# Kernel tuning notes

Hardware: AMD Instinct MI355X
Metric: run time of the kernel (lower is better)

Reference implementation:

```python
import jax, jax.numpy as jnp
import numpy as np

TOKEN_DIM = 1024
HIDDEN = 256
NUM_FREQS = 10
FOURIER_DIM = 3 * (2 * NUM_FREQS + 1)  # include_input + sin/cos per freq = 63
EPS_LN = 1e-5
EPS_NORM = 1e-12


def fourier_encode(x):
    # x: [..., 3] -> [..., 3*(1+2*NUM_FREQS)]
    freqs = (2.0 ** jnp.arange(NUM_FREQS)).astype(x.dtype)  # [F]
    xf = x[..., None] * freqs  # [..., 3, F]
    sin = jnp.sin(xf)
    cos = jnp.cos(xf)
    enc = jnp.concatenate([x[..., None], sin, cos], axis=-1)  # [..., 3, 1+2F]
    return enc.reshape(*x.shape[:-1], FOURIER_DIM)


def layer_norm(x, g, b):
    mu = jnp.mean(x, axis=-1, keepdims=True)
    var = jnp.mean((x - mu) ** 2, axis=-1, keepdims=True)
    return (x - mu) * jax.lax.rsqrt(var + EPS_LN) * g + b


def setup_inputs() -> dict:
    key = jax.random.key(0)
    ks = jax.random.split(key, 12)
    B, T, N = 2, 512, 40000
    in_dim = TOKEN_DIM + FOURIER_DIM
    s1 = 1.0 / np.sqrt(in_dim)
    s2 = 1.0 / np.sqrt(HIDDEN)
    return {
        "transformer_tokens": jax.random.normal(ks[0], (B, T, TOKEN_DIM), jnp.float32),
        "scaffold_anchors": jax.random.normal(ks[1], (B, T, 3), jnp.float32),
        "scaffold_token_ids": jax.random.randint(ks[2], (B, N), 0, T, jnp.int32),
        "W1": jax.random.uniform(ks[3], (in_dim, HIDDEN), jnp.float32, -s1, s1),
        "b1": jnp.zeros((HIDDEN,), jnp.float32),
        "g1": jnp.ones((HIDDEN,), jnp.float32),
        "be1": jnp.zeros((HIDDEN,), jnp.float32),
        "W2": jax.random.uniform(ks[4], (HIDDEN, HIDDEN), jnp.float32, -s2, s2),
        "b2": jnp.zeros((HIDDEN,), jnp.float32),
        "g2": jnp.ones((HIDDEN,), jnp.float32),
        "be2": jnp.zeros((HIDDEN,), jnp.float32),
        "W3": jax.random.uniform(ks[5], (HIDDEN, 14), jnp.float32, -s2, s2),
        "b3": jnp.zeros((14,), jnp.float32),
    }


def reference(transformer_tokens, scaffold_anchors, scaffold_token_ids,
              W1, b1, g1, be1, W2, b2, g2, be2, W3, b3):
    B, T, D = transformer_tokens.shape
    N = scaffold_token_ids.shape[1]
    idx = scaffold_token_ids.astype(jnp.int32)
    # Gather per-Gaussian anchors and token features: [B, N, 3] / [B, N, D]
    per_anchor = jnp.take_along_axis(scaffold_anchors, idx[..., None], axis=1)
    token_feats = jnp.take_along_axis(transformer_tokens, idx[..., None], axis=1)
    spatial_enc = fourier_encode(per_anchor)  # [B, N, FOURIER_DIM]
    combined = jnp.concatenate([token_feats, spatial_enc], axis=-1)
    h = jax.nn.relu(layer_norm(combined @ W1 + b1, g1, be1))
    h = jax.nn.relu(layer_norm(h @ W2 + b2, g2, be2))
    raw = h @ W3 + b3  # [B, N, 14]
    pos = raw[..., 0:3]
    color = jnp.clip(raw[..., 3:6], 0.0, 1.0)
    opac = jax.nn.sigmoid(raw[..., 6:7])
    scale = jnp.exp(raw[..., 7:10])
    q = raw[..., 10:14]
    qn = jnp.linalg.norm(q, axis=-1, keepdims=True)
    quat = q / jnp.maximum(qn, EPS_NORM)
    out = jnp.concatenate([pos, color, opac, scale, quat], axis=-1)
    return out.reshape(B, N * 14)
```

## Files before the change

kernel.cpp:

```cpp
#include <hip/hip_runtime.h>

#define TDIM   1024
#define HID    256
#define FDIM   63
#define INDIM  1087
#define TT     512
#define NBATCH 2
#define NROWS  1024
#define KSPLIT 4
#define KCHUNK 272
#define EPS_LN   1e-5f
#define EPS_NORM 1e-12f

#define FMA4(A, s, W)                                   \
    (A).x = fmaf((s), (W).x, (A).x);                    \
    (A).y = fmaf((s), (W).y, (A).y);                    \
    (A).z = fmaf((s), (W).z, (A).z);                    \
    (A).w = fmaf((s), (W).w, (A).w)

__device__ __forceinline__ float wave_reduce_sum(float v) {
    #pragma unroll
    for (int m = 32; m >= 1; m >>= 1) v += __shfl_xor(v, m);
    return v;
}

__device__ __forceinline__ float fourier_val(const float* __restrict__ anchors, int row, int u) {
    const int c = u / 21;
    const int w = u % 21;
    const float x = anchors[row * 3 + c];
    if (w == 0)  return x;
    if (w <= 10) return sinf(x * (float)(1u << (w - 1)));
    return cosf(x * (float)(1u << (w - 11)));
}

__global__ __launch_bounds__(512) void stage1_partial_kernel(
    const float* __restrict__ tokens,
    const float* __restrict__ anchors,
    const float* __restrict__ W1,
    float* __restrict__ part)
{
    const int tid    = threadIdx.x;
    const int rt     = blockIdx.x >> 2;
    const int z      = blockIdx.x & 3;
    const int kstart = z * KCHUNK;
    const int kcount = min(KCHUNK, INDIM - kstart);
    const int wave   = tid >> 6;
    const int c4     = (tid & 63) << 2;
    const int row0   = rt * 16 + wave * 2;

    const float* __restrict__ t0p = tokens + (size_t)(row0 + 0) * TDIM;
    const float* __restrict__ t1p = tokens + (size_t)(row0 + 1) * TDIM;

    float4 acc0 = {0.f, 0.f, 0.f, 0.f};
    float4 acc1 = acc0;

    const int glim = kcount >> 2;
    const int gtok = (kstart < TDIM) ? min(glim, (TDIM - kstart) >> 2) : 0;

    #pragma unroll 4
    for (int g = 0; g < gtok; ++g) {
        const int k = kstart + (g << 2);
        const float4 w0 = *(const float4*)&W1[(size_t)(k + 0) * HID + c4];
        const float4 w1 = *(const float4*)&W1[(size_t)(k + 1) * HID + c4];
        const float4 w2 = *(const float4*)&W1[(size_t)(k + 2) * HID + c4];
        const float4 w3 = *(const float4*)&W1[(size_t)(k + 3) * HID + c4];
        const float4 s0 = *(const float4*)&t0p[k];
        const float4 s1 = *(const float4*)&t1p[k];
        FMA4(acc0, s0.x, w0); FMA4(acc0, s0.y, w1); FMA4(acc0, s0.z, w2); FMA4(acc0, s0.w, w3);
        FMA4(acc1, s1.x, w0); FMA4(acc1, s1.y, w1); FMA4(acc1, s1.z, w2); FMA4(acc1, s1.w, w3);
    }

    for (int g = gtok; g < glim; ++g) {
        const int k = kstart + (g << 2);
        const float4 w0 = *(const float4*)&W1[(size_t)(k + 0) * HID + c4];
        const float4 w1 = *(const float4*)&W1[(size_t)(k + 1) * HID + c4];
        const float4 w2 = *(const float4*)&W1[(size_t)(k + 2) * HID + c4];
        const float4 w3 = *(const float4*)&W1[(size_t)(k + 3) * HID + c4];
        const int u = k - TDIM;
        float4 s0, s1;
        s0.x = fourier_val(anchors, row0 + 0, u);     s0.y = fourier_val(anchors, row0 + 0, u + 1);
        s0.z = fourier_val(anchors, row0 + 0, u + 2); s0.w = fourier_val(anchors, row0 + 0, u + 3);
        s1.x = fourier_val(anchors, row0 + 1, u);     s1.y = fourier_val(anchors, row0 + 1, u + 1);
        s1.z = fourier_val(anchors, row0 + 1, u + 2); s1.w = fourier_val(anchors, row0 + 1, u + 3);
        FMA4(acc0, s0.x, w0); FMA4(acc0, s0.y, w1); FMA4(acc0, s0.z, w2); FMA4(acc0, s0.w, w3);
        FMA4(acc1, s1.x, w0); FMA4(acc1, s1.y, w1); FMA4(acc1, s1.z, w2); FMA4(acc1, s1.w, w3);
    }

    for (int k = kstart + (glim << 2); k < kstart + kcount; ++k) {
        const float4 w = *(const float4*)&W1[(size_t)k * HID + c4];
        const float v0 = (k < TDIM) ? t0p[k] : fourier_val(anchors, row0 + 0, k - TDIM);
        const float v1 = (k < TDIM) ? t1p[k] : fourier_val(anchors, row0 + 1, k - TDIM);
        FMA4(acc0, v0, w); FMA4(acc1, v1, w);
    }

    float* __restrict__ pb = part + (size_t)z * NROWS * HID;
    *(float4*)&pb[(size_t)(row0 + 0) * HID + c4] = acc0;
    *(float4*)&pb[(size_t)(row0 + 1) * HID + c4] = acc1;
}

__global__ __launch_bounds__(256) void decode_tail_kernel(
    const float* __restrict__ part,
    const float* __restrict__ b1,
    const float* __restrict__ g1,
    const float* __restrict__ be1,
    const float* __restrict__ W2,
    const float* __restrict__ b2,
    const float* __restrict__ g2,
    const float* __restrict__ be2,
    const float* __restrict__ W3,
    const float* __restrict__ b3,
    float* __restrict__ decoded)
{
    __shared__ float h1[4][HID];
    __shared__ float h2[4][HID];
    __shared__ float raws[4][16];

    const int tid  = threadIdx.x;
    const int wave = tid >> 6;
    const int lane = tid & 63;
    const int row  = blockIdx.x * 4 + wave;

    {
        const size_t off = (size_t)row * HID;
        float x0 = b1[lane], x1 = b1[lane + 64], x2 = b1[lane + 128], x3 = b1[lane + 192];
        #pragma unroll
        for (int zz = 0; zz < KSPLIT; ++zz) {
            const float* __restrict__ p = part + (size_t)zz * NROWS * HID + off;
            x0 += p[lane]; x1 += p[lane + 64]; x2 += p[lane + 128]; x3 += p[lane + 192];
        }
        const float ga0 = g1[lane], ga1 = g1[lane + 64], ga2 = g1[lane + 128], ga3 = g1[lane + 192];
        const float bb0 = be1[lane], bb1 = be1[lane + 64], bb2 = be1[lane + 128], bb3 = be1[lane + 192];
        const float s  = wave_reduce_sum(x0 + x1 + x2 + x3);
        const float mu = s * (1.0f / 256.0f);
        const float d0 = x0 - mu, d1 = x1 - mu, d2 = x2 - mu, d3 = x3 - mu;
        const float sq = wave_reduce_sum(d0 * d0 + d1 * d1 + d2 * d2 + d3 * d3);
        const float rstd = 1.0f / sqrtf(sq * (1.0f / 256.0f) + EPS_LN);
        h1[wave][lane]       = fmaxf(0.0f, fmaf(d0 * rstd, ga0, bb0));
        h1[wave][lane + 64]  = fmaxf(0.0f, fmaf(d1 * rstd, ga1, bb1));
        h1[wave][lane + 128] = fmaxf(0.0f, fmaf(d2 * rstd, ga2, bb2));
        h1[wave][lane + 192] = fmaxf(0.0f, fmaf(d3 * rstd, ga3, bb3));
    }
    __syncthreads();

    {
        const int cc = lane << 2;
        float4 acc = *(const float4*)&b2[cc];
        #pragma unroll 4
        for (int k = 0; k < HID; k += 4) {
            const float4 hk = *(const float4*)&h1[wave][k];
            const float4 w0 = *(const float4*)&W2[(size_t)(k + 0) * HID + cc];
            const float4 w1 = *(const float4*)&W2[(size_t)(k + 1) * HID + cc];
            const float4 w2 = *(const float4*)&W2[(size_t)(k + 2) * HID + cc];
            const float4 w3 = *(const float4*)&W2[(size_t)(k + 3) * HID + cc];
            FMA4(acc, hk.x, w0); FMA4(acc, hk.y, w1); FMA4(acc, hk.z, w2); FMA4(acc, hk.w, w3);
        }
        *(float4*)&h2[wave][cc] = acc;
    }
    __syncthreads();

    {
        float x0 = h2[wave][lane], x1 = h2[wave][lane + 64], x2 = h2[wave][lane + 128], x3 = h2[wave][lane + 192];
        const float ga0 = g2[lane], ga1 = g2[lane + 64], ga2 = g2[lane + 128], ga3 = g2[lane + 192];
        const float bb0 = be2[lane], bb1 = be2[lane + 64], bb2 = be2[lane + 128], bb3 = be2[lane + 192];
        const float s  = wave_reduce_sum(x0 + x1 + x2 + x3);
        const float mu = s * (1.0f / 256.0f);
        const float d0 = x0 - mu, d1 = x1 - mu, d2 = x2 - mu, d3 = x3 - mu;
        const float sq = wave_reduce_sum(d0 * d0 + d1 * d1 + d2 * d2 + d3 * d3);
        const float rstd = 1.0f / sqrtf(sq * (1.0f / 256.0f) + EPS_LN);
        h2[wave][lane]       = fmaxf(0.0f, fmaf(d0 * rstd, ga0, bb0));
        h2[wave][lane + 64]  = fmaxf(0.0f, fmaf(d1 * rstd, ga1, bb1));
        h2[wave][lane + 128] = fmaxf(0.0f, fmaf(d2 * rstd, ga2, bb2));
        h2[wave][lane + 192] = fmaxf(0.0f, fmaf(d3 * rstd, ga3, bb3));
    }
    __syncthreads();

    if (tid < 4 * 14) {
        const int r = tid / 14;
        const int m = tid % 14;
        float a = b3[m];
        #pragma unroll 4
        for (int k = 0; k < HID; ++k) a = fmaf(h2[r][k], W3[k * 14 + m], a);
        raws[r][m] = a;
    }
    __syncthreads();

    if (tid < 4 * 14) {
        const int r = tid / 14;
        const int m = tid % 14;
        const float x = raws[r][m];
        float v;
        if (m < 3) {
            v = x;
        } else if (m < 6) {
            v = fminf(fmaxf(x, 0.0f), 1.0f);
        } else if (m == 6) {
            v = 1.0f / (1.0f + expf(-x));
        } else if (m < 10) {
            v = expf(x);
        } else {
            const float q0 = raws[r][10], q1 = raws[r][11];
            const float q2 = raws[r][12], q3 = raws[r][13];
            const float nrm = sqrtf(q0 * q0 + q1 * q1 + q2 * q2 + q3 * q3);
            v = x / fmaxf(nrm, EPS_NORM);
        }
        decoded[(size_t)(blockIdx.x * 4 + r) * 14 + m] = v;
    }
}

__global__ __launch_bounds__(256) void gather_kernel(
    const int* __restrict__ ids,
    const float* __restrict__ decoded,
    float* __restrict__ out,
    int N, int total14)
{
    const int j = blockIdx.x * blockDim.x + threadIdx.x;
    if (j >= total14) return;
    const int i = j / 14;
    const int k = j - i * 14;
    const int b = (i >= N) ? 1 : 0;
    const int t = ids[i];
    out[j] = decoded[(size_t)(b * TT + t) * 14 + k];
}

extern "C" void kernel_launch(void* const* d_in, const int* in_sizes, int n_in,
                              void* d_out, int out_size, void* d_ws, size_t ws_size,
                              hipStream_t stream) {
    const float* tokens  = (const float*)d_in[0];
    const float* anchors = (const float*)d_in[1];
    const int*   ids     = (const int*)d_in[2];
    const float* W1  = (const float*)d_in[3];
    const float* b1  = (const float*)d_in[4];
    const float* g1  = (const float*)d_in[5];
    const float* be1 = (const float*)d_in[6];
    const float* W2  = (const float*)d_in[7];
    const float* b2  = (const float*)d_in[8];
    const float* g2  = (const float*)d_in[9];
    const float* be2 = (const float*)d_in[10];
    const float* W3  = (const float*)d_in[11];
    const float* b3  = (const float*)d_in[12];

    float* decoded = (float*)d_ws;
    float* part    = (float*)d_out;
    float* out     = (float*)d_out;

    const int N = in_sizes[2] / NBATCH;

    stage1_partial_kernel<<<64 * KSPLIT, 512, 0, stream>>>(tokens, anchors, W1, part);

    decode_tail_kernel<<<NROWS / 4, 256, 0, stream>>>(
        part, b1, g1, be1, W2, b2, g2, be2, W3, b3, decoded);

    const int total14 = NBATCH * N * 14;
    gather_kernel<<<(total14 + 255) / 256, 256, 0, stream>>>(ids, decoded, out, N, total14);
}
```

Baseline: 163.6 us.

## Split stage1 across more blocks and parallelize W3 projection with wave reductions

Stage1 now runs 1024 smaller blocks (256 threads, 8 rows, half the hidden columns each) instead of 256 blocks of 512 threads, using float2 accumulators, to spread the work over more CUs. The W3 output projection in the tail kernel moves from 56 serial threads each looping over 256 terms to all 256 threads computing partial dot products followed by wave reductions. The extra parallelism costs more redundant token loads per block and 14 shuffle reductions per wave.

```diff
diff --git a/kernel.cpp b/kernel.cpp
--- a/kernel.cpp
+++ b/kernel.cpp
@@ -18,6 +18,10 @@
     (A).z = fmaf((s), (W).z, (A).z);                    \
     (A).w = fmaf((s), (W).w, (A).w)
 
+#define FMA2(A, s, W)                                   \
+    (A).x = fmaf((s), (W).x, (A).x);                    \
+    (A).y = fmaf((s), (W).y, (A).y)
+
 __device__ __forceinline__ float wave_reduce_sum(float v) {
     #pragma unroll
     for (int m = 32; m >= 1; m >>= 1) v += __shfl_xor(v, m);
@@ -33,26 +37,30 @@
     return cosf(x * (float)(1u << (w - 11)));
 }
 
-__global__ __launch_bounds__(512) void stage1_partial_kernel(
+__global__ __launch_bounds__(256) void stage1_partial_kernel(
     const float* __restrict__ tokens,
     const float* __restrict__ anchors,
     const float* __restrict__ W1,
     float* __restrict__ part)
 {
-    const int tid    = threadIdx.x;
-    const int rt     = blockIdx.x >> 2;
-    const int z      = blockIdx.x & 3;
+    const int tid  = threadIdx.x;
+    const int bid  = blockIdx.x;
+    const int z    = bid & 3;
+    const int cg   = (bid >> 2) & 1;
+    const int rt   = bid >> 3;
+    const int wave = tid >> 6;
+    const int lane = tid & 63;
+    const int c2   = (cg << 7) + (lane << 1);
+    const int row0 = rt * 8 + wave * 2;
+
     const int kstart = z * KCHUNK;
     const int kcount = min(KCHUNK, INDIM - kstart);
-    const int wave   = tid >> 6;
-    const int c4     = (tid & 63) << 2;
-    const int row0   = rt * 16 + wave * 2;
 
     const float* __restrict__ t0p = tokens + (size_t)(row0 + 0) * TDIM;
     const float* __restrict__ t1p = tokens + (size_t)(row0 + 1) * TDIM;
 
-    float4 acc0 = {0.f, 0.f, 0.f, 0.f};
-    float4 acc1 = acc0;
+    float2 acc0 = {0.f, 0.f};
+    float2 acc1 = acc0;
 
     const int glim = kcount >> 2;
     const int gtok = (kstart < TDIM) ? min(glim, (TDIM - kstart) >> 2) : 0;
@@ -60,42 +68,42 @@
     #pragma unroll 4
     for (int g = 0; g < gtok; ++g) {
         const int k = kstart + (g << 2);
-        const float4 w0 = *(const float4*)&W1[(size_t)(k + 0) * HID + c4];
-        const float4 w1 = *(const float4*)&W1[(size_t)(k + 1) * HID + c4];
-        const float4 w2 = *(const float4*)&W1[(size_t)(k + 2) * HID + c4];
-        const float4 w3 = *(const float4*)&W1[(size_t)(k + 3) * HID + c4];
+        const float2 w0 = *(const float2*)&W1[(size_t)(k + 0) * HID + c2];
+        const float2 w1 = *(const float2*)&W1[(size_t)(k + 1) * HID + c2];
+        const float2 w2 = *(const float2*)&W1[(size_t)(k + 2) * HID + c2];
+        const float2 w3 = *(const float2*)&W1[(size_t)(k + 3) * HID + c2];
         const float4 s0 = *(const float4*)&t0p[k];
         const float4 s1 = *(const float4*)&t1p[k];
-        FMA4(acc0, s0.x, w0); FMA4(acc0, s0.y, w1); FMA4(acc0, s0.z, w2); FMA4(acc0, s0.w, w3);
-        FMA4(acc1, s1.x, w0); FMA4(acc1, s1.y, w1); FMA4(acc1, s1.z, w2); FMA4(acc1, s1.w, w3);
+        FMA2(acc0, s0.x, w0); FMA2(acc0, s0.y, w1); FMA2(acc0, s0.z, w2); FMA2(acc0, s0.w, w3);
+        FMA2(acc1, s1.x, w0); FMA2(acc1, s1.y, w1); FMA2(acc1, s1.z, w2); FMA2(acc1, s1.w, w3);
     }
 
     for (int g = gtok; g < glim; ++g) {
         const int k = kstart + (g << 2);
-        const float4 w0 = *(const float4*)&W1[(size_t)(k + 0) * HID + c4];
-        const float4 w1 = *(const float4*)&W1[(size_t)(k + 1) * HID + c4];
-        const float4 w2 = *(const float4*)&W1[(size_t)(k + 2) * HID + c4];
-        const float4 w3 = *(const float4*)&W1[(size_t)(k + 3) * HID + c4];
+        const float2 w0 = *(const float2*)&W1[(size_t)(k + 0) * HID + c2];
+        const float2 w1 = *(const float2*)&W1[(size_t)(k + 1) * HID + c2];
+        const float2 w2 = *(const float2*)&W1[(size_t)(k + 2) * HID + c2];
+        const float2 w3 = *(const float2*)&W1[(size_t)(k + 3) * HID + c2];
         const int u = k - TDIM;
         float4 s0, s1;
         s0.x = fourier_val(anchors, row0 + 0, u);     s0.y = fourier_val(anchors, row0 + 0, u + 1);
         s0.z = fourier_val(anchors, row0 + 0, u + 2); s0.w = fourier_val(anchors, row0 + 0, u + 3);
         s1.x = fourier_val(anchors, row0 + 1, u);     s1.y = fourier_val(anchors, row0 + 1, u + 1);
         s1.z = fourier_val(anchors, row0 + 1, u + 2); s1.w = fourier_val(anchors, row0 + 1, u + 3);
-        FMA4(acc0, s0.x, w0); FMA4(acc0, s0.y, w1); FMA4(acc0, s0.z, w2); FMA4(acc0, s0.w, w3);
-        FMA4(acc1, s1.x, w0); FMA4(acc1, s1.y, w1); FMA4(acc1, s1.z, w2); FMA4(acc1, s1.w, w3);
+        FMA2(acc0, s0.x, w0); FMA2(acc0, s0.y, w1); FMA2(acc0, s0.z, w2); FMA2(acc0, s0.w, w3);
+        FMA2(acc1, s1.x, w0); FMA2(acc1, s1.y, w1); FMA2(acc1, s1.z, w2); FMA2(acc1, s1.w, w3);
     }
 
     for (int k = kstart + (glim << 2); k < kstart + kcount; ++k) {
-        const float4 w = *(const float4*)&W1[(size_t)k * HID + c4];
+        const float2 w = *(const float2*)&W1[(size_t)k * HID + c2];
         const float v0 = (k < TDIM) ? t0p[k] : fourier_val(anchors, row0 + 0, k - TDIM);
         const float v1 = (k < TDIM) ? t1p[k] : fourier_val(anchors, row0 + 1, k - TDIM);
-        FMA4(acc0, v0, w); FMA4(acc1, v1, w);
+        FMA2(acc0, v0, w); FMA2(acc1, v1, w);
     }
 
     float* __restrict__ pb = part + (size_t)z * NROWS * HID;
-    *(float4*)&pb[(size_t)(row0 + 0) * HID + c4] = acc0;
-    *(float4*)&pb[(size_t)(row0 + 1) * HID + c4] = acc1;
+    *(float2*)&pb[(size_t)(row0 + 0) * HID + c2] = acc0;
+    *(float2*)&pb[(size_t)(row0 + 1) * HID + c2] = acc1;
 }
 
 __global__ __launch_bounds__(256) void decode_tail_kernel(
@@ -174,13 +182,20 @@
     }
     __syncthreads();
 
-    if (tid < 4 * 14) {
-        const int r = tid / 14;
-        const int m = tid % 14;
-        float a = b3[m];
-        #pragma unroll 4
-        for (int k = 0; k < HID; ++k) a = fmaf(h2[r][k], W3[k * 14 + m], a);
-        raws[r][m] = a;
+    {
+        const float hk0 = h2[wave][lane];
+        const float hk1 = h2[wave][lane + 64];
+        const float hk2 = h2[wave][lane + 128];
+        const float hk3 = h2[wave][lane + 192];
+        #pragma unroll
+        for (int m = 0; m < 14; ++m) {
+            float p = hk0 * W3[lane * 14 + m]
+                    + hk1 * W3[(lane + 64) * 14 + m]
+                    + hk2 * W3[(lane + 128) * 14 + m]
+                    + hk3 * W3[(lane + 192) * 14 + m];
+            p = wave_reduce_sum(p);
+            if (lane == m) raws[wave][m] = p + b3[m];
+        }
     }
     __syncthreads();
 
@@ -245,7 +260,7 @@
 
     const int N = in_sizes[2] / NBATCH;
 
-    stage1_partial_kernel<<<64 * KSPLIT, 512, 0, stream>>>(tokens, anchors, W1, part);
+    stage1_partial_kernel<<<128 * 2 * KSPLIT, 256, 0, stream>>>(tokens, anchors, W1, part);
 
     decode_tail_kernel<<<NROWS / 4, 256, 0, stream>>>(
         part, b1, g1, be1, W2, b2, g2, be2, W3, b3, decoded);
```

Result: slower. 174.1 us (+6.4%).
